# Performance work log

Measured on AMD Instinct MI355X. Metric: run time of the kernel, lower is better.

The kernel has to match this reference:

```python
import jax, jax.numpy as jnp
import numpy as np

NV = [12544, 6272, 3136, 1568, 784]  # vertex counts, fine -> coarse
SPIRAL = 9


def _grid_sample(im, grid):
    """Faithful port of the hand-rolled bilinear_grid_sample, align_corners=True.
    im: (n, c, h, w); grid: (n, gh, gw, 2) in [-1, 1]. Returns (n, c, gh*gw)."""
    n, c, h, w = im.shape
    gx = grid[..., 0].reshape(n, -1)
    gy = grid[..., 1].reshape(n, -1)
    x = (gx + 1) / 2 * (w - 1)
    y = (gy + 1) / 2 * (h - 1)
    x0 = jnp.floor(x); y0 = jnp.floor(y)
    x1 = x0 + 1; y1 = y0 + 1
    wa = (x1 - x) * (y1 - y)
    wb = (x1 - x) * (y - y0)
    wc = (x - x0) * (y1 - y)
    wd = (x - x0) * (y - y0)
    imp = jnp.pad(im, ((0, 0), (0, 0), (1, 1), (1, 1)))  # explicit zero pad as in source
    ph, pw = h + 2, w + 2
    x0i = jnp.clip(x0.astype(jnp.int32) + 1, 0, pw - 1)
    x1i = jnp.clip(x1.astype(jnp.int32) + 1, 0, pw - 1)
    y0i = jnp.clip(y0.astype(jnp.int32) + 1, 0, ph - 1)
    y1i = jnp.clip(y1.astype(jnp.int32) + 1, 0, ph - 1)
    impf = imp.reshape(n, c, -1)

    def gat(xi, yi):
        idx = xi + yi * pw  # (n, P)
        return jnp.take_along_axis(impf, idx[:, None, :], axis=2)  # (n, c, P)

    Ia = gat(x0i, y0i); Ib = gat(x0i, y1i); Ic = gat(x1i, y0i); Id = gat(x1i, y1i)
    return Ia * wa[:, None] + Ib * wb[:, None] + Ic * wc[:, None] + Id * wd[:, None]


def _pool(x, col, val):
    """Mesh up-pooling: gather columns, weight, and 3-way sum per output vertex.
    With row = repeat(arange(n_out), 3) the row_map built in __init__ is exactly
    arange(3*n_out).reshape(n_out, 3), so the three gathers reduce to reshape+sum."""
    out = x[:, col, :] * val[None, :, None]  # (B, 3*n_out, C)
    n_out = val.shape[0] // 3
    return out.reshape(x.shape[0], n_out, 3, x.shape[2]).sum(axis=2)


def _dsconv(x, idx, dw, pw):
    """Depthwise-separable spiral conv: gather spiral neighborhood, depthwise
    conv over spiral dim (per-channel), then 1x1 pointwise projection."""
    gsp = x[:, idx, :]                        # (B, N, S, Cin)
    y = jnp.einsum('bnsc,cs->bnc', gsp, dw)   # depthwise over spiral
    return y @ pw                             # (B, N, Cout)


def setup_inputs() -> dict:
    key = jax.random.key(0)
    ks = jax.random.split(key, 32)
    d = {}
    d['uv'] = jax.random.uniform(ks[0], (16, 64, 2), jnp.float32)
    d['feat'] = jax.random.normal(ks[1], (16, 256, 4, 4), jnp.float32)
    d['upsample'] = jax.random.normal(ks[2], (NV[4], 64), jnp.float32) * 0.01
    chs = [(256, 256), (256, 256), (256, 128), (128, 64)]
    for i, (ci, co) in enumerate(chs):
        d['dw%d' % i] = jax.random.normal(ks[3 + 2 * i], (ci, SPIRAL), jnp.float32) * (1.0 / SPIRAL)
        d['pw%d' % i] = jax.random.normal(ks[4 + 2 * i], (ci, co), jnp.float32) * (ci ** -0.5)
    d['dw_head'] = jax.random.normal(ks[11], (64, SPIRAL), jnp.float32) * (1.0 / SPIRAL)
    d['pw_head'] = jax.random.normal(ks[12], (64, 3), jnp.float32) * (64 ** -0.5)
    for j in range(4):
        n_out, n_in = NV[j], NV[j + 1]
        d['sp_idx_%d' % j] = jax.random.randint(ks[13 + j], (NV[j], SPIRAL), 0, NV[j], dtype=jnp.int32)
        d['up_col_%d' % j] = jax.random.randint(ks[17 + j], (3 * n_out,), 0, n_in, dtype=jnp.int32)
        d['up_val_%d' % j] = jax.random.uniform(ks[21 + j], (3 * n_out,), jnp.float32)
    return d


def reference(uv, feat, upsample, dw0, pw0, dw1, pw1, dw2, pw2, dw3, pw3, dw_head, pw_head,
              up_val_0, up_val_1, up_val_2, up_val_3,
              sp_idx_0, sp_idx_1, sp_idx_2, sp_idx_3,
              up_col_0, up_col_1, up_col_2, up_col_3):
    g = jnp.clip((uv - 0.5) * 2.0, -1.0, 1.0)[:, :, None, :]  # (B, P, 1, 2)
    x = _grid_sample(feat, g)            # (B, 256, P)
    x = x.transpose(0, 2, 1)             # (B, P, 256)
    x = jnp.einsum('vp,bpc->bvc', upsample, x)  # (B, 784, 256) coarse mesh feats
    specs = [(up_col_3, up_val_3, sp_idx_3, dw0, pw0),
             (up_col_2, up_val_2, sp_idx_2, dw1, pw1),
             (up_col_1, up_val_1, sp_idx_1, dw2, pw2),
             (up_col_0, up_val_0, sp_idx_0, dw3, pw3)]
    for col, val, idx, dw, pw in specs:
        x = _pool(x, col, val)
        x = jax.nn.relu(_dsconv(x, idx, dw, pw))
    return _dsconv(x, sp_idx_0, dw_head, pw_head)  # (B, 12544, 3)
```

## Files before the change

### kernel.cpp

```cpp
#include <hip/hip_runtime.h>


typedef _Float16 half8 __attribute__((ext_vector_type(8)));
typedef float    f32x4 __attribute__((ext_vector_type(4)));

__device__ __forceinline__ float4 ld4(const float* p) { return *(const float4*)p; }

__device__ __forceinline__ float lo16f(unsigned u) {
  _Float16 h; unsigned short s = (unsigned short)(u & 0xffffu);
  __builtin_memcpy(&h, &s, 2); return (float)h;
}
__device__ __forceinline__ float hi16f(unsigned u) {
  _Float16 h; unsigned short s = (unsigned short)(u >> 16);
  __builtin_memcpy(&h, &s, 2); return (float)h;
}
__device__ __forceinline__ float h2f(unsigned short s) {
  _Float16 h; __builtin_memcpy(&h, &s, 2); return (float)h;
}
__device__ __forceinline__ unsigned short hbits(float v) {
  _Float16 h = (_Float16)v; unsigned short u; __builtin_memcpy(&u, &h, 2); return u;
}
__device__ __forceinline__ unsigned pk2h(float a, float b) {
  return (unsigned)hbits(a) | ((unsigned)hbits(b) << 16);
}
__device__ __forceinline__ void split2h(float v, unsigned short& h, unsigned short& l) {
  _Float16 hf = (_Float16)v;
  float hif = (float)hf;
  _Float16 lf = (_Float16)((v - hif) * 2048.0f);
  __builtin_memcpy(&h, &hf, 2); __builtin_memcpy(&l, &lf, 2);
}
__device__ __forceinline__ void gload_lds16(const unsigned short* g, unsigned short* l) {
  __builtin_amdgcn_global_load_lds(
      (const __attribute__((address_space(1))) unsigned int*)g,
      (__attribute__((address_space(3))) unsigned int*)l, 16, 0, 0);
}

__global__ __launch_bounds__(256) void k_prep(
    const float* __restrict__ pw0, const float* __restrict__ pw1,
    const float* __restrict__ pw2, const float* __restrict__ pw3,
    unsigned short* __restrict__ dst)
{
  const int b = blockIdx.x, t = threadIdx.x;
  const float* src; int ci_sh, co, f, off;
  if (b < 256)      { src = pw0; ci_sh = 8; co = 256; f = b*256 + t;       off = 0; }
  else if (b < 512) { src = pw1; ci_sh = 8; co = 256; f = (b-256)*256 + t; off = 65536; }
  else if (b < 640) { src = pw2; ci_sh = 8; co = 128; f = (b-512)*256 + t; off = 131072; }
  else              { src = pw3; ci_sh = 7; co = 64;  f = (b-640)*256 + t; off = 163840; }
  const int n = f >> ci_sh, k = f & ((1 << ci_sh) - 1);
  float v = src[(size_t)k*co + n];
  unsigned short h, l; split2h(v, h, l);
  dst[off + f]          = h;
  dst[172032 + off + f] = l;
}

__global__ __launch_bounds__(256) void k_prep_head(
    const float* __restrict__ dwh, const float* __restrict__ pwh,
    unsigned short* __restrict__ dst)
{
  const int i = blockIdx.x*256 + threadIdx.x;
  const int n = i >> 6, c = i & 63;
  float v = 0.f;
  if (n < 27) v = dwh[c*9 + n/3] * pwh[c*3 + n%3];
  unsigned short h, l; split2h(v, h, l);
  dst[i] = h; dst[2048 + i] = l;
}

__global__ __launch_bounds__(256) void k_prep_dw(
    const float* __restrict__ dw0, const float* __restrict__ dw1,
    const float* __restrict__ dw2, const float* __restrict__ dw3,
    float* __restrict__ dst)
{
  const int i = blockIdx.x*256 + threadIdx.x;
  if (i >= 8064) return;
  const float* src; int rel, C, off;
  if (i < 2304)      { src = dw0; rel = i;        C = 256; off = 0; }
  else if (i < 4608) { src = dw1; rel = i - 2304; C = 256; off = 2304; }
  else if (i < 6912) { src = dw2; rel = i - 4608; C = 256; off = 4608; }
  else               { src = dw3; rel = i - 6912; C = 128; off = 6912; }
  const int s = rel / C, c = rel % C;
  dst[off + rel] = src[c*9 + s];
}

__global__ __launch_bounds__(256) void k_samp(
    const float* __restrict__ uv, const float* __restrict__ feat,
    unsigned short* __restrict__ xs)
{
  __shared__ float feat_l[256][17];
  const int tid = threadIdx.x;
  const int b   = blockIdx.x;

  const float* fr = feat + ((size_t)b*256 + tid)*16;
  #pragma unroll
  for (int i = 0; i < 16; i += 4) {
    float4 f = ld4(fr + i);
    feat_l[tid][i+0] = f.x; feat_l[tid][i+1] = f.y;
    feat_l[tid][i+2] = f.z; feat_l[tid][i+3] = f.w;
  }
  #pragma unroll 4
  for (int p = 0; p < 64; ++p) {
    float gx = uv[((size_t)b*64 + p)*2 + 0];
    float gy = uv[((size_t)b*64 + p)*2 + 1];
    gx = fminf(fmaxf((gx - 0.5f)*2.f, -1.f), 1.f);
    gy = fminf(fmaxf((gy - 0.5f)*2.f, -1.f), 1.f);
    float x = (gx + 1.f)*0.5f*3.f;
    float y = (gy + 1.f)*0.5f*3.f;
    float fx = floorf(x), fy = floorf(y);
    int ix0 = (int)fx, iy0 = (int)fy;
    float wx = x - fx, wy = y - fy;
    int ix1 = ix0 + 1 > 3 ? 3 : ix0 + 1;
    int iy1 = iy0 + 1 > 3 ? 3 : iy0 + 1;
    float v00 = feat_l[tid][iy0*4+ix0];
    float v01 = feat_l[tid][iy0*4+ix1];
    float v10 = feat_l[tid][iy1*4+ix0];
    float v11 = feat_l[tid][iy1*4+ix1];
    float xv = (1.f-wy)*((1.f-wx)*v00 + wx*v01) + wy*((1.f-wx)*v10 + wx*v11);
    xs[((size_t)b*64 + p)*256 + tid] = hbits(xv);
  }
}

__global__ __launch_bounds__(256) void k_up(
    const unsigned short* __restrict__ xs, const float* __restrict__ up,
    unsigned short* __restrict__ x0)
{
  const int tid = threadIdx.x;
  const int b   = blockIdx.y;
  const int v0  = blockIdx.x * 16;

  float acc[16];
  #pragma unroll
  for (int i = 0; i < 16; ++i) acc[i] = 0.f;

  #pragma unroll 8
  for (int p = 0; p < 64; ++p) {
    const float xv = h2f(xs[((size_t)b*64 + p)*256 + tid]);
    #pragma unroll
    for (int i = 0; i < 16; ++i)
      acc[i] += up[(size_t)(v0+i)*64 + p] * xv;
  }
  #pragma unroll
  for (int i = 0; i < 16; ++i)
    x0[((size_t)b*784 + v0 + i)*256 + tid] = hbits(acc[i]);
}

template<int C>
__global__ __launch_bounds__(256) void k_pool(
    const unsigned short* __restrict__ x, const int* __restrict__ col,
    const float* __restrict__ val, unsigned short* __restrict__ out,
    int Vin, int Vout)
{
  constexpr int KGc = C/8;
  constexpr int UPB = 2*KGc;
  const int bp = blockIdx.x & 7;
  const int v0 = (blockIdx.x >> 3) * 8;
  const int t  = threadIdx.x;

  #pragma unroll
  for (int i = 0; i < (8*UPB)/256; ++i) {
    const int id = t + i*256;
    const int vl = id / UPB;
    const int rem = id - vl*UPB;
    const int bl = rem / KGc;
    const int kg = rem - bl*KGc;
    const int v  = v0 + vl;
    const int b  = 2*bp + bl;
    const int c0 = col[3*v+0], c1 = col[3*v+1], c2 = col[3*v+2];
    const float w0 = val[3*v+0], w1 = val[3*v+1], w2 = val[3*v+2];
    const uint4 A = *(const uint4*)(x + ((size_t)b*Vin + c0)*C + 8*kg);
    const uint4 B = *(const uint4*)(x + ((size_t)b*Vin + c1)*C + 8*kg);
    const uint4 Cv= *(const uint4*)(x + ((size_t)b*Vin + c2)*C + 8*kg);
    uint4 R;
    R.x = pk2h(w0*lo16f(A.x)+w1*lo16f(B.x)+w2*lo16f(Cv.x),
               w0*hi16f(A.x)+w1*hi16f(B.x)+w2*hi16f(Cv.x));
    R.y = pk2h(w0*lo16f(A.y)+w1*lo16f(B.y)+w2*lo16f(Cv.y),
               w0*hi16f(A.y)+w1*hi16f(B.y)+w2*hi16f(Cv.y));
    R.z = pk2h(w0*lo16f(A.z)+w1*lo16f(B.z)+w2*lo16f(Cv.z),
               w0*hi16f(A.z)+w1*hi16f(B.z)+w2*hi16f(Cv.z));
    R.w = pk2h(w0*lo16f(A.w)+w1*lo16f(B.w)+w2*lo16f(Cv.w),
               w0*hi16f(A.w)+w1*hi16f(B.w)+w2*hi16f(Cv.w));
    *(uint4*)(out + ((size_t)b*Vout + v)*C + 8*kg) = R;
  }
}

template<int CI>
__global__ __launch_bounds__(256) void k_dw(
    const unsigned short* __restrict__ pin, const int* __restrict__ idx,
    const float* __restrict__ dwT, unsigned short* __restrict__ aout,
    int Vin, int VG)
{
  constexpr int KG    = CI/8;
  constexpr int SLOTS = 256/KG;
  constexpr int VPB   = 2*SLOTS;

  const int t     = threadIdx.x;
  const int xcd   = blockIdx.x & 7;
  const int i     = blockIdx.x >> 3;
  const int phase = (i >= VG) ? 1 : 0;
  const int vg    = i - phase*VG;
  const int b     = xcd + 8*phase;
  const int kg    = t & (KG - 1);
  const int slot  = t / KG;
  const int va    = vg*VPB + slot;
  const int vb2   = va + SLOTS;

  const unsigned short* base = pin + (size_t)b*Vin*CI + 8*kg;
  float y0[8], y1[8];
  #pragma unroll
  for (int j = 0; j < 8; ++j) { y0[j] = 0.f; y1[j] = 0.f; }

  #pragma unroll
  for (int s = 0; s < 9; ++s) {
    const float4 wa = *(const float4*)(dwT + s*CI + 8*kg);
    const float4 wb = *(const float4*)(dwT + s*CI + 8*kg + 4);
    const uint4 g0 = *(const uint4*)(base + (size_t)idx[va *9 + s]*CI);
    const uint4 g1 = *(const uint4*)(base + (size_t)idx[vb2*9 + s]*CI);
    y0[0] += wa.x*lo16f(g0.x); y0[1] += wa.y*hi16f(g0.x);
    y0[2] += wa.z*lo16f(g0.y); y0[3] += wa.w*hi16f(g0.y);
    y0[4] += wb.x*lo16f(g0.z); y0[5] += wb.y*hi16f(g0.z);
    y0[6] += wb.z*lo16f(g0.w); y0[7] += wb.w*hi16f(g0.w);
    y1[0] += wa.x*lo16f(g1.x); y1[1] += wa.y*hi16f(g1.x);
    y1[2] += wa.z*lo16f(g1.y); y1[3] += wa.w*hi16f(g1.y);
    y1[4] += wb.x*lo16f(g1.z); y1[5] += wb.y*hi16f(g1.z);
    y1[6] += wb.z*lo16f(g1.w); y1[7] += wb.w*hi16f(g1.w);
  }
  uint4 p0, p1;
  p0.x = pk2h(y0[0], y0[1]); p0.y = pk2h(y0[2], y0[3]);
  p0.z = pk2h(y0[4], y0[5]); p0.w = pk2h(y0[6], y0[7]);
  p1.x = pk2h(y1[0], y1[1]); p1.y = pk2h(y1[2], y1[3]);
  p1.z = pk2h(y1[4], y1[5]); p1.w = pk2h(y1[6], y1[7]);
  *(uint4*)(aout + (size_t)(va *16 + b)*CI + 8*kg) = p0;
  *(uint4*)(aout + (size_t)(vb2*16 + b)*CI + 8*kg) = p1;
}

template<int CI, int COT, int NTW, bool RELU>
__global__ __launch_bounds__(256) void k_gemm(
    const unsigned short* __restrict__ A,
    const unsigned short* __restrict__ bhp, const unsigned short* __restrict__ blp,
    unsigned short* __restrict__ out, int Vout)
{
  constexpr int CHUNKS = CI/32;
  constexpr int NCOL   = NTW*64;
  constexpr int OROW   = NCOL + 8;
  constexpr int ABYTES = 64*CI*2;
  constexpr int OBYTES = 64*OROW*2;
  constexpr int LBYTES = (ABYTES > OBYTES) ? ABYTES : OBYTES;
  constexpr int SLOTS  = ABYTES/16;

  __shared__ __align__(16) char lds_raw[LBYTES];
  unsigned short* a_l = (unsigned short*)lds_raw;

  const int t  = threadIdx.x;
  const size_t m0 = (size_t)blockIdx.x * 64;
  const int co0 = blockIdx.y * NCOL;
  const int w = t >> 6, l = t & 15, q = (t >> 4) & 3;
  const int lane6 = t & 63;

  #pragma unroll
  for (int r = 0; r < SLOTS/256; ++r) {
    const int s    = t + r*256;
    const int c    = s >> 8;
    const int mt   = (s >> 6) & 3;
    const int ql   = s & 63;
    const int m    = mt*16 + (ql & 15);
    const int koff = c*32 + (ql >> 4)*8;
    gload_lds16(A + (m0 + m)*CI + koff, a_l + (size_t)s*8);
  }
  __syncthreads();

  f32x4 ah[4][NTW], ax[4][NTW];
  #pragma unroll
  for (int mt = 0; mt < 4; ++mt)
    #pragma unroll
    for (int n = 0; n < NTW; ++n)
      #pragma unroll
      for (int r = 0; r < 4; ++r) { ah[mt][n][r] = 0.f; ax[mt][n][r] = 0.f; }

  #pragma unroll
  for (int c = 0; c < CHUNKS; ++c) {
    const int k0 = c*32 + q*8;
    half8 fa[4], fbh[NTW], fbl[NTW];
    #pragma unroll
    for (int mt = 0; mt < 4; ++mt)
      fa[mt] = *(const half8*)(a_l + (size_t)(c*256 + mt*64 + lane6)*8);
    #pragma unroll
    for (int n = 0; n < NTW; ++n) {
      const size_t boff = (size_t)(co0 + (w*NTW + n)*16 + l)*CI + k0;
      fbh[n] = *(const half8*)(bhp + boff);
      fbl[n] = *(const half8*)(blp + boff);
    }
    #pragma unroll
    for (int mt = 0; mt < 4; ++mt)
      #pragma unroll
      for (int n = 0; n < NTW; ++n) {
        ah[mt][n] = __builtin_amdgcn_mfma_f32_16x16x32_f16(fa[mt], fbh[n], ah[mt][n], 0, 0, 0);
        ax[mt][n] = __builtin_amdgcn_mfma_f32_16x16x32_f16(fa[mt], fbl[n], ax[mt][n], 0, 0, 0);
      }
  }

  __syncthreads();
  unsigned short (*ot)[OROW] = (unsigned short (*)[OROW])lds_raw;
  #pragma unroll
  for (int mt = 0; mt < 4; ++mt)
    #pragma unroll
    for (int n = 0; n < NTW; ++n) {
      const int colg = (w*NTW + n)*16 + l;
      #pragma unroll
      for (int r = 0; r < 4; ++r) {
        const int row = mt*16 + q*4 + r;
        float v = ah[mt][n][r] + ax[mt][n][r] * (1.0f/2048.0f);
        if (RELU) v = fmaxf(v, 0.f);
        ot[row][colg] = hbits(v);
      }
    }
  __syncthreads();
  constexpr int PR = NCOL/8;
  #pragma unroll
  for (int i = 0; i < (64*PR)/256; ++i) {
    const int item = t + i*256;
    const int r  = item / PR;
    const int cp = (item % PR)*8;
    const size_t m = m0 + r;
    const int v = (int)(m >> 4), b = (int)(m & 15);
    *(uint4*)(out + ((size_t)b*Vout + v)*COT + co0 + cp) = *(const uint4*)&ot[r][cp];
  }
}

__global__ __launch_bounds__(256) void k_headz(
    const unsigned short* __restrict__ A,
    const unsigned short* __restrict__ bhT, const unsigned short* __restrict__ blT,
    float* __restrict__ z)
{
  __shared__ float zt[4][32][16];

  const int t = threadIdx.x;
  const size_t m0 = (size_t)blockIdx.x * 64;
  const int w = t >> 6, l = t & 15, q = (t >> 4) & 3;

  f32x4 acch[2], accl[2];
  #pragma unroll
  for (int n = 0; n < 2; ++n)
    #pragma unroll
    for (int r = 0; r < 4; ++r) { acch[n][r] = 0.f; accl[n][r] = 0.f; }

  const size_t m = m0 + w*16 + l;
  const size_t arow = ((m & 15)*12544 + (m >> 4))*64;
  #pragma unroll
  for (int c = 0; c < 2; ++c) {
    const int k0 = c*32 + q*8;
    half8 fa = *(const half8*)(A + arow + k0);
    #pragma unroll
    for (int n = 0; n < 2; ++n) {
      half8 fbh = *(const half8*)(bhT + (size_t)(n*16 + l)*64 + k0);
      half8 fbl = *(const half8*)(blT + (size_t)(n*16 + l)*64 + k0);
      acch[n] = __builtin_amdgcn_mfma_f32_16x16x32_f16(fa, fbh, acch[n], 0, 0, 0);
      accl[n] = __builtin_amdgcn_mfma_f32_16x16x32_f16(fa, fbl, accl[n], 0, 0, 0);
    }
  }

  #pragma unroll
  for (int n = 0; n < 2; ++n)
    #pragma unroll
    for (int r = 0; r < 4; ++r)
      zt[w][n*16 + l][q*4 + r] = acch[n][r] + accl[n][r] * (1.0f/2048.0f);
  __syncthreads();

  const size_t u0 = m0 >> 4;
  #pragma unroll
  for (int i = 0; i < 7; ++i) {
    const int item = t + i*256;
    if (item < 1728) {
      const int ul  = item / 432;
      const int rem = item - ul*432;
      const int s   = rem / 48;
      const int bj  = rem - s*48;
      const int b   = bj / 3;
      const int j   = bj - b*3;
      z[(u0 + ul)*432 + rem] = zt[ul][s*3 + j][b];
    }
  }
}

__global__ __launch_bounds__(256) void k_head2(
    const float* __restrict__ z, const int* __restrict__ idx,
    float* __restrict__ out, int nvert)
{
  const int w    = threadIdx.x >> 6;
  const int lane = threadIdx.x & 63;
  const int v    = blockIdx.x*4 + w;
  if (lane < 48) {
    float acc = 0.f;
    #pragma unroll
    for (int s = 0; s < 9; ++s) {
      const int u = idx[v*9 + s];
      acc += z[(size_t)u*432 + s*48 + lane];
    }
    const int b = lane / 3, j = lane - b*3;
    out[((size_t)b*nvert + v)*3 + j] = acc;
  }
}

extern "C" void kernel_launch(void* const* d_in, const int* in_sizes, int n_in,
                              void* d_out, int out_size, void* d_ws, size_t ws_size,
                              hipStream_t stream)
{
  const float* uv   = (const float*)d_in[0];
  const float* feat = (const float*)d_in[1];
  const float* up   = (const float*)d_in[2];
  const float* dw0  = (const float*)d_in[3];
  const float* pw0  = (const float*)d_in[4];
  const float* dw1  = (const float*)d_in[5];
  const float* pw1  = (const float*)d_in[6];
  const float* dw2  = (const float*)d_in[7];
  const float* pw2  = (const float*)d_in[8];
  const float* dw3  = (const float*)d_in[9];
  const float* pw3  = (const float*)d_in[10];
  const float* dwh  = (const float*)d_in[11];
  const float* pwh  = (const float*)d_in[12];
  const int*   sp0  = (const int*)d_in[13];
  const int*   col0 = (const int*)d_in[14];
  const float* val0 = (const float*)d_in[15];
  const int*   sp1  = (const int*)d_in[16];
  const int*   col1 = (const int*)d_in[17];
  const float* val1 = (const float*)d_in[18];
  const int*   sp2  = (const int*)d_in[19];
  const int*   col2 = (const int*)d_in[20];
  const float* val2 = (const float*)d_in[21];
  const int*   sp3  = (const int*)d_in[22];
  const int*   col3 = (const int*)d_in[23];
  const float* val3 = (const float*)d_in[24];

  unsigned short* bufA  = (unsigned short*)d_ws;
  unsigned short* bufB  = (unsigned short*)((char*)d_ws + 25690112);
  unsigned short* bufC  = (unsigned short*)((char*)d_ws + 77070336);
  unsigned short* pwT   = (unsigned short*)((char*)d_ws + 128450560);
  unsigned short* bhead = (unsigned short*)((char*)d_ws + 129138688);
  float*          dwT   = (float*)((char*)d_ws + 129155072);
  float*          zbuf  = (float*)((char*)d_ws + 129187328);
  unsigned short* xs    = (unsigned short*)((char*)d_ws + 150863360);
  float* outp = (float*)d_out;

  unsigned short* h0 = pwT;            unsigned short* L0 = pwT + 172032;
  unsigned short* h1 = pwT + 65536;    unsigned short* L1 = L0 + 65536;
  unsigned short* h2 = pwT + 131072;   unsigned short* L2 = L0 + 131072;
  unsigned short* h3 = pwT + 163840;   unsigned short* L3 = L0 + 163840;
  unsigned short* hh = bhead;          unsigned short* Lh = bhead + 2048;
  float* dwT0 = dwT;          float* dwT1 = dwT + 2304;
  float* dwT2 = dwT + 4608;   float* dwT3 = dwT + 6912;

  k_prep<<<672, 256, 0, stream>>>(pw0, pw1, pw2, pw3, pwT);
  k_prep_head<<<8, 256, 0, stream>>>(dwh, pwh, bhead);
  k_prep_dw<<<32, 256, 0, stream>>>(dw0, dw1, dw2, dw3, dwT);
  k_samp<<<16, 256, 0, stream>>>(uv, feat, xs);
  k_up<<<dim3(49,16,1), 256, 0, stream>>>(xs, up, bufA);

  k_pool<256><<<1568, 256, 0, stream>>>(bufA, col3, val3, bufB, 784, 1568);
  k_dw<256><<<16*98, 256, 0, stream>>>(bufB, sp3, dwT0, bufC, 1568, 98);
  k_gemm<256,256,2,true><<<dim3(392,2), 256, 0, stream>>>(bufC, h0, L0, bufA, 1568);

  k_pool<256><<<3136, 256, 0, stream>>>(bufA, col2, val2, bufB, 1568, 3136);
  k_dw<256><<<16*196, 256, 0, stream>>>(bufB, sp2, dwT1, bufC, 3136, 196);
  k_gemm<256,256,2,true><<<dim3(784,2), 256, 0, stream>>>(bufC, h1, L1, bufA, 3136);

  k_pool<256><<<6272, 256, 0, stream>>>(bufA, col1, val1, bufB, 3136, 6272);
  k_dw<256><<<16*392, 256, 0, stream>>>(bufB, sp1, dwT2, bufC, 6272, 392);
  k_gemm<256,128,2,true><<<dim3(1568,1), 256, 0, stream>>>(bufC, h2, L2, bufA, 6272);

  k_pool<128><<<12544, 256, 0, stream>>>(bufA, col0, val0, bufB, 6272, 12544);
  k_dw<128><<<16*392, 256, 0, stream>>>(bufB, sp0, dwT3, bufC, 12544, 392);
  k_gemm<128,64,1,true><<<dim3(3136,1), 256, 0, stream>>>(bufC, h3, L3, bufA, 12544);

  k_headz<<<3136, 256, 0, stream>>>(bufA, hh, Lh, zbuf);
  k_head2<<<3136, 256, 0, stream>>>(zbuf, sp0, outp, 12544);
}
```

Before: 422.0 us.

## Make GEMM blocks persistent over multiple M-tiles with double-buffered LDS staging

Each k_gemm block now processes T consecutive 64-row tiles instead of one, prefetching the next tile's A operand into a second LDS buffer while the current tile runs its MFMAs. The output staging reuses the current A buffer. The aim is to overlap global-to-LDS loads with compute and cut block launch overhead. In exchange it adds extra barriers per tile, doubles LDS use (lower occupancy), and shrinks the grid, which may leave CUs underused for the smaller layers.

```diff
diff --git a/kernel.cpp b/kernel.cpp
--- a/kernel.cpp
+++ b/kernel.cpp
@@ -235,92 +235,107 @@
 __global__ __launch_bounds__(256) void k_gemm(
     const unsigned short* __restrict__ A,
     const unsigned short* __restrict__ bhp, const unsigned short* __restrict__ blp,
-    unsigned short* __restrict__ out, int Vout)
+    unsigned short* __restrict__ out, int Vout, int T)
 {
   constexpr int CHUNKS = CI/32;
   constexpr int NCOL   = NTW*64;
   constexpr int OROW   = NCOL + 8;
   constexpr int ABYTES = 64*CI*2;
-  constexpr int OBYTES = 64*OROW*2;
-  constexpr int LBYTES = (ABYTES > OBYTES) ? ABYTES : OBYTES;
   constexpr int SLOTS  = ABYTES/16;
-
-  __shared__ __align__(16) char lds_raw[LBYTES];
-  unsigned short* a_l = (unsigned short*)lds_raw;
-
-  const int t  = threadIdx.x;
-  const size_t m0 = (size_t)blockIdx.x * 64;
-  const int co0 = blockIdx.y * NCOL;
+  constexpr int AUS    = SLOTS*8;
+
+  __shared__ __align__(16) unsigned short a_l[2*AUS];
+
+  const int t    = threadIdx.x;
+  const int co0  = blockIdx.y * NCOL;
   const int w = t >> 6, l = t & 15, q = (t >> 4) & 3;
   const int lane6 = t & 63;
-
-  #pragma unroll
-  for (int r = 0; r < SLOTS/256; ++r) {
-    const int s    = t + r*256;
-    const int c    = s >> 8;
-    const int mt   = (s >> 6) & 3;
-    const int ql   = s & 63;
-    const int m    = mt*16 + (ql & 15);
-    const int koff = c*32 + (ql >> 4)*8;
-    gload_lds16(A + (m0 + m)*CI + koff, a_l + (size_t)s*8);
-  }
+  const int tix0 = blockIdx.x * T;
+
+  auto stage = [&](int tix, int sel) {
+    const size_t m0 = (size_t)tix * 64;
+    unsigned short* dst = a_l + (size_t)sel*AUS;
+    #pragma unroll
+    for (int r = 0; r < SLOTS/256; ++r) {
+      const int s    = t + r*256;
+      const int c    = s >> 8;
+      const int mt   = (s >> 6) & 3;
+      const int ql   = s & 63;
+      const int m    = mt*16 + (ql & 15);
+      const int koff = c*32 + (ql >> 4)*8;
+      gload_lds16(A + (m0 + m)*CI + koff, dst + (size_t)s*8);
+    }
+  };
+
+  stage(tix0, 0);
   __syncthreads();
 
-  f32x4 ah[4][NTW], ax[4][NTW];
-  #pragma unroll
-  for (int mt = 0; mt < 4; ++mt)
-    #pragma unroll
-    for (int n = 0; n < NTW; ++n)
+  for (int j = 0; j < T; ++j) {
+    const int tix = tix0 + j;
+    const int sel = j & 1;
+    if (j + 1 < T) stage(tix + 1, sel ^ 1);
+
+    const unsigned short* ab = a_l + (size_t)sel*AUS;
+    f32x4 ah[4][NTW], ax[4][NTW];
+    #pragma unroll
+    for (int mt = 0; mt < 4; ++mt)
       #pragma unroll
-      for (int r = 0; r < 4; ++r) { ah[mt][n][r] = 0.f; ax[mt][n][r] = 0.f; }
-
-  #pragma unroll
-  for (int c = 0; c < CHUNKS; ++c) {
-    const int k0 = c*32 + q*8;
-    half8 fa[4], fbh[NTW], fbl[NTW];
-    #pragma unroll
-    for (int mt = 0; mt < 4; ++mt)
-      fa[mt] = *(const half8*)(a_l + (size_t)(c*256 + mt*64 + lane6)*8);
-    #pragma unroll
-    for (int n = 0; n < NTW; ++n) {
-      const size_t boff = (size_t)(co0 + (w*NTW + n)*16 + l)*CI + k0;
-      fbh[n] = *(const half8*)(bhp + boff);
-      fbl[n] = *(const half8*)(blp + boff);
-    }
+      for (int n = 0; n < NTW; ++n)
+        #pragma unroll
+        for (int r = 0; r < 4; ++r) { ah[mt][n][r] = 0.f; ax[mt][n][r] = 0.f; }
+
+    #pragma unroll
+    for (int c = 0; c < CHUNKS; ++c) {
+      const int k0 = c*32 + q*8;
+      half8 fa[4], fbh[NTW], fbl[NTW];
+      #pragma unroll
+      for (int mt = 0; mt < 4; ++mt)
+        fa[mt] = *(const half8*)(ab + (size_t)(c*256 + mt*64 + lane6)*8);
+      #pragma unroll
+      for (int n = 0; n < NTW; ++n) {
+        const size_t boff = (size_t)(co0 + (w*NTW + n)*16 + l)*CI + k0;
+        fbh[n] = *(const half8*)(bhp + boff);
+        fbl[n] = *(const half8*)(blp + boff);
+      }
+      #pragma unroll
+      for (int mt = 0; mt < 4; ++mt)
+        #pragma unroll
+        for (int n = 0; n < NTW; ++n) {
+          ah[mt][n] = __builtin_amdgcn_mfma_f32_16x16x32_f16(fa[mt], fbh[n], ah[mt][n], 0, 0, 0);
+          ax[mt][n] = __builtin_amdgcn_mfma_f32_16x16x32_f16(fa[mt], fbl[n], ax[mt][n], 0, 0, 0);
+        }
+    }
+
+    __syncthreads();
+
+    unsigned short (*ot)[OROW] = (unsigned short (*)[OROW])(a_l + (size_t)sel*AUS);
     #pragma unroll
     for (int mt = 0; mt < 4; ++mt)
       #pragma unroll
       for (int n = 0; n < NTW; ++n) {
-        ah[mt][n] = __builtin_amdgcn_mfma_f32_16x16x32_f16(fa[mt], fbh[n], ah[mt][n], 0, 0, 0);
-        ax[mt][n] = __builtin_amdgcn_mfma_f32_16x16x32_f16(fa[mt], fbl[n], ax[mt][n], 0, 0, 0);
+        const int colg = (w*NTW + n)*16 + l;
+        #pragma unroll
+        for (int r = 0; r < 4; ++r) {
+          const int row = mt*16 + q*4 + r;
+          float v = ah[mt][n][r] + ax[mt][n][r] * (1.0f/2048.0f);
+          if (RELU) v = fmaxf(v, 0.f);
+          ot[row][colg] = hbits(v);
+        }
       }
-  }
-
-  __syncthreads();
-  unsigned short (*ot)[OROW] = (unsigned short (*)[OROW])lds_raw;
-  #pragma unroll
-  for (int mt = 0; mt < 4; ++mt)
-    #pragma unroll
-    for (int n = 0; n < NTW; ++n) {
-      const int colg = (w*NTW + n)*16 + l;
-      #pragma unroll
-      for (int r = 0; r < 4; ++r) {
-        const int row = mt*16 + q*4 + r;
-        float v = ah[mt][n][r] + ax[mt][n][r] * (1.0f/2048.0f);
-        if (RELU) v = fmaxf(v, 0.f);
-        ot[row][colg] = hbits(v);
-      }
-    }
-  __syncthreads();
-  constexpr int PR = NCOL/8;
-  #pragma unroll
-  for (int i = 0; i < (64*PR)/256; ++i) {
-    const int item = t + i*256;
-    const int r  = item / PR;
-    const int cp = (item % PR)*8;
-    const size_t m = m0 + r;
-    const int v = (int)(m >> 4), b = (int)(m & 15);
-    *(uint4*)(out + ((size_t)b*Vout + v)*COT + co0 + cp) = *(const uint4*)&ot[r][cp];
+    __syncthreads();
+
+    constexpr int PR = NCOL/8;
+    const size_t m0 = (size_t)tix * 64;
+    #pragma unroll
+    for (int i = 0; i < (64*PR)/256; ++i) {
+      const int item = t + i*256;
+      const int r  = item / PR;
+      const int cp = (item % PR)*8;
+      const size_t m = m0 + r;
+      const int v = (int)(m >> 4), b = (int)(m & 15);
+      *(uint4*)(out + ((size_t)b*Vout + v)*COT + co0 + cp) = *(const uint4*)&ot[r][cp];
+    }
+    __syncthreads();
   }
 }
 
@@ -454,19 +469,19 @@
 
   k_pool<256><<<1568, 256, 0, stream>>>(bufA, col3, val3, bufB, 784, 1568);
   k_dw<256><<<16*98, 256, 0, stream>>>(bufB, sp3, dwT0, bufC, 1568, 98);
-  k_gemm<256,256,2,true><<<dim3(392,2), 256, 0, stream>>>(bufC, h0, L0, bufA, 1568);
+  k_gemm<256,256,2,true><<<dim3(196,2), 256, 0, stream>>>(bufC, h0, L0, bufA, 1568, 2);
 
   k_pool<256><<<3136, 256, 0, stream>>>(bufA, col2, val2, bufB, 1568, 3136);
   k_dw<256><<<16*196, 256, 0, stream>>>(bufB, sp2, dwT1, bufC, 3136, 196);
-  k_gemm<256,256,2,true><<<dim3(784,2), 256, 0, stream>>>(bufC, h1, L1, bufA, 3136);
+  k_gemm<256,256,2,true><<<dim3(392,2), 256, 0, stream>>>(bufC, h1, L1, bufA, 3136, 2);
 
   k_pool<256><<<6272, 256, 0, stream>>>(bufA, col1, val1, bufB, 3136, 6272);
   k_dw<256><<<16*392, 256, 0, stream>>>(bufB, sp1, dwT2, bufC, 6272, 392);
-  k_gemm<256,128,2,true><<<dim3(1568,1), 256, 0, stream>>>(bufC, h2, L2, bufA, 6272);
+  k_gemm<256,128,2,true><<<dim3(392,1), 256, 0, stream>>>(bufC, h2, L2, bufA, 6272, 4);
 
   k_pool<128><<<12544, 256, 0, stream>>>(bufA, col0, val0, bufB, 6272, 12544);
   k_dw<128><<<16*392, 256, 0, stream>>>(bufB, sp0, dwT3, bufC, 12544, 392);
-  k_gemm<128,64,1,true><<<dim3(3136,1), 256, 0, stream>>>(bufC, h3, L3, bufA, 12544);
+  k_gemm<128,64,1,true><<<dim3(784,1), 256, 0, stream>>>(bufC, h3, L3, bufA, 12544, 4);
 
   k_headz<<<3136, 256, 0, stream>>>(bufA, hh, Lh, zbuf);
   k_head2<<<3136, 256, 0, stream>>>(zbuf, sp0, outp, 12544);
```

After: 413.3 us. 1.02x faster.
